# Kernel optimization log

Hardware: AMD Instinct MI355X
Metric: run time of the kernel (lower is better)

## Reference

```python
import jax, jax.numpy as jnp
import numpy as np

FULL_SCALE = 128.0
R = 0.5
TOPK = 4


def setup_inputs() -> dict:
    key = jax.random.key(0)
    k0, k1, k2, k3, k4 = jax.random.split(key, 5)
    B, Na, Nb, D = 16, 2048, 2048, 512
    coords_a = jax.random.randint(k0, (B, Na, 3), 0, 128, dtype=jnp.int32)
    coords_b = jax.random.randint(k1, (B, Nb, 3), 0, 128, dtype=jnp.int32)
    feats_a = jax.random.normal(k2, (B, Na, D), jnp.float32)
    feats_b = jax.random.normal(k3, (B, Nb, D), jnp.float32)
    W = jax.random.normal(k4, (2 * D, D), jnp.float32) / np.sqrt(2 * D).astype(np.float32)
    bias = jnp.zeros((D,), jnp.float32)
    return {"feats_a": feats_a, "feats_b": feats_b, "W": W, "bias": bias,
            "coords_a": coords_a, "coords_b": coords_b}


def _pairwise_l2(ca, cb):
    # ca: [B,Na,3], cb: [B,Nb,3] -> [B,Na,Nb], scaled by full_scale
    x2 = jnp.sum(ca * ca, axis=-1)[:, :, None]
    y2 = jnp.sum(cb * cb, axis=-1)[:, None, :]
    sq = x2 + y2 - 2.0 * jnp.einsum('bnd,bmd->bnm', ca, cb)
    return jnp.sqrt(jnp.clip(sq, 0.0, None)) / FULL_SCALE


def reference(feats_a, feats_b, W, bias, coords_a, coords_b):
    ca = coords_a.astype(jnp.float32)
    cb = coords_b.astype(jnp.float32)
    dist = _pairwise_l2(ca, cb)                       # [B,Na,Nb]
    neg_top, idx = jax.lax.top_k(-dist, TOPK)         # smallest TOPK distances
    dist_w = R - jnp.clip(-neg_top, 0.0, R)           # [B,Na,k]
    # gather neighbor features: [B,Na,k,D]
    b_f = jnp.take_along_axis(feats_b[:, None, :, :], idx[:, :, :, None], axis=2)
    a_f = feats_a[:, :, None, :]                      # broadcast over k
    h = jnp.concatenate([b_f, a_f - b_f], axis=-1)    # [B,Na,k,2D]
    fused = jnp.sum(jax.nn.relu(h @ W + bias) * dist_w[..., None], axis=2)  # [B,Na,D]
    # ME.cat(a, tmp): concatenate features along channel dim
    return jnp.concatenate([feats_a, fused], axis=-1)  # [B,Na,2D]
```

## Files before the change

kernel.cpp:

```cpp
#include <hip/hip_runtime.h>
#include <hip/hip_bf16.h>
#include <cstdint>
#include <cstddef>

#define NA   2048
#define NB   2048
#define DD   512

typedef __attribute__((ext_vector_type(8))) short bf16x8;
typedef __attribute__((ext_vector_type(4))) float f32x4;
typedef unsigned short u16;
typedef unsigned int   u32;

__device__ __forceinline__ u16 f2b_hw(float f) {
    u32 w;
    asm("v_cvt_pk_bf16_f32 %0, %1, %2" : "=v"(w) : "v"(f), "v"(f));
    return (u16)w;
}
__device__ __forceinline__ float b2f(u16 h) {
    return __uint_as_float(((u32)h) << 16);
}
__device__ __forceinline__ u32 umin32(u32 a, u32 b) { return a < b ? a : b; }
__device__ __forceinline__ u32 umax32(u32 a, u32 b) { return a > b ? a : b; }
__device__ __forceinline__ u32 med3u(u32 a, u32 b, u32 c) {
    return umax32(umin32(a, b), umin32(umax32(a, b), c));
}
__device__ __forceinline__ bf16x8 cvt8(f32x4 v0, f32x4 v1) {
    u32 w0, w1, w2, w3;
    asm("v_cvt_pk_bf16_f32 %0, %1, %2" : "=v"(w0) : "v"(v0[0]), "v"(v0[1]));
    asm("v_cvt_pk_bf16_f32 %0, %1, %2" : "=v"(w1) : "v"(v0[2]), "v"(v0[3]));
    asm("v_cvt_pk_bf16_f32 %0, %1, %2" : "=v"(w2) : "v"(v1[0]), "v"(v1[1]));
    asm("v_cvt_pk_bf16_f32 %0, %1, %2" : "=v"(w3) : "v"(v1[2]), "v"(v1[3]));
    union { u32 u[4]; bf16x8 v; } cv;
    cv.u[0] = w0; cv.u[1] = w1; cv.u[2] = w2; cv.u[3] = w3;
    return cv.v;
}

#define GLDS16(gsrc, ldst)                                                  \
    __builtin_amdgcn_global_load_lds(                                       \
        (const __attribute__((address_space(1))) void*)(gsrc),              \
        (__attribute__((address_space(3))) void*)(ldst), 16, 0, 0)

__global__ __launch_bounds__(256) void prep_w(const float* __restrict__ W,
                                              u16* __restrict__ W2T,
                                              u16* __restrict__ WdT) {
    __shared__ float s2[64][65];
    __shared__ float sd[64][65];
    int kb = blockIdx.x * 64, nb = blockIdx.y * 64;
    int tid = threadIdx.x;
    int c = tid & 63, r0 = tid >> 6;
    #pragma unroll
    for (int p = 0; p < 16; ++p) {
        int r = p * 4 + r0;
        float w1 = W[(size_t)(kb + r) * DD + nb + c];
        float w2 = W[(size_t)(512 + kb + r) * DD + nb + c];
        s2[r][c] = w2;
        sd[r][c] = w1 - w2;
    }
    __syncthreads();
    #pragma unroll
    for (int p = 0; p < 16; ++p) {
        int n = p * 4 + r0;
        W2T[(size_t)(nb + n) * DD + kb + c] = f2b_hw(s2[c][n]);
        WdT[(size_t)(nb + n) * DD + kb + c] = f2b_hw(sd[c][n]);
    }
}

__global__ __launch_bounds__(512) void topk_kernel(const int* __restrict__ ca,
                                                   const int* __restrict__ cb,
                                                   int* __restrict__ idx_out,
                                                   float* __restrict__ w_out) {
    __shared__ u32 pcb[NB];
    __shared__ u32 part[3 * 128 * 4];
    int b = blockIdx.y;
    int tid = threadIdx.x;
    for (int p = tid; p < NB; p += 512) {
        const int* c = cb + ((size_t)b * NB + p) * 3;
        pcb[p] = (u32)c[0] | ((u32)c[1] << 8) | ((u32)c[2] << 16);
    }
    __syncthreads();

    int q = tid & 127, g = tid >> 7;
    int i = blockIdx.x * 128 + q;
    const int* ac = ca + ((size_t)b * NA + i) * 3;
    int ax = ac[0], ay = ac[1], az = ac[2];

    u32 k0 = ~0u, k1 = ~0u, k2 = ~0u, k3 = ~0u;
    int j0 = g * 512;
    #pragma unroll 8
    for (int jj = 0; jj < 512; ++jj) {
        int j = j0 + jj;
        u32 p = pcb[j];
        int dx = ax - (int)(p & 255u);
        int dy = ay - (int)((p >> 8) & 255u);
        int dz = az - (int)(p >> 16);
        u32 s = (u32)(__mul24(dx, dx) + __mul24(dy, dy) + __mul24(dz, dz));
        u32 key = (s << 11) | (u32)j;
        u32 nk0 = umin32(k0, key);
        u32 nk1 = med3u(key, k0, k1);
        u32 nk2 = med3u(key, k1, k2);
        u32 nk3 = med3u(key, k2, k3);
        k0 = nk0; k1 = nk1; k2 = nk2; k3 = nk3;
    }
    if (g) {
        u32* pp = &part[((g - 1) * 128 + q) * 4];
        pp[0] = k0; pp[1] = k1; pp[2] = k2; pp[3] = k3;
    }
    __syncthreads();
    if (g == 0) {
        #pragma unroll
        for (int L = 0; L < 3; ++L) {
            const u32* pp = &part[(L * 128 + q) * 4];
            #pragma unroll
            for (int t = 0; t < 4; ++t) {
                u32 key = pp[t];
                u32 nk0 = umin32(k0, key);
                u32 nk1 = med3u(key, k0, k1);
                u32 nk2 = med3u(key, k1, k2);
                u32 nk3 = med3u(key, k2, k3);
                k0 = nk0; k1 = nk1; k2 = nk2; k3 = nk3;
            }
        }
        size_t o = ((size_t)b * NA + i) * 4;
        u32 ks[4] = {k0, k1, k2, k3};
        #pragma unroll
        for (int t = 0; t < 4; ++t) {
            idx_out[o + t] = (int)(ks[t] & 2047u);
            float d = sqrtf((float)(ks[t] >> 11)) * (1.0f / 128.0f);
            w_out[o + t] = 0.5f - fminf(d, 0.5f);
        }
    }
}

template<bool FUSED>
__global__ __launch_bounds__(256, 1) void gemm_kernel(
    const float* __restrict__ A, const u16* __restrict__ BT,
    u16* __restrict__ C, const int* __restrict__ idxb,
    const float* __restrict__ wb, const float* __restrict__ bias,
    const u16* __restrict__ Qb, float* __restrict__ out) {

    __shared__ __align__(16) char smem[FUSED ? 66560 : 65536];

    const int tid  = threadIdx.x;
    const int lane = tid & 63;
    const int wave = tid >> 6;
    const int mb   = blockIdx.x;
    const int m0   = FUSED ? ((((mb & 7) << 5) | (mb >> 3)) << 7) : (mb << 7);
    const int n0   = blockIdx.y << 8;
    const int l15  = lane & 15;
    const int fq   = lane >> 4;
    const int wr   = (wave >> 1) << 6;
    const int wc   = (wave & 1) << 7;

    int aflat[4]; const float* asp[4];
    #pragma unroll
    for (int i = 0; i < 4; ++i) {
        int flat = i * 256 + tid;
        int row = flat >> 3, pq = flat & 7;
        aflat[i] = flat;
        asp[i] = A + (size_t)(m0 + row) * DD + ((pq ^ (row & 7)) << 2);
    }
    int bflat[4]; const u16* bsp[4];
    #pragma unroll
    for (int i = 0; i < 4; ++i) {
        int flat = i * 256 + tid;
        int row = flat >> 2, pq = flat & 3;
        bflat[i] = flat;
        bsp[i] = BT + (size_t)(n0 + row) * DD + ((pq ^ ((row >> 1) & 3)) << 3);
    }

    int aoff[4][2], boff[8];
    #pragma unroll
    for (int mf = 0; mf < 4; ++mf) {
        int R = wr + mf * 16 + l15;
        aoff[mf][0] = R * 128 + (((2 * fq) ^ (R & 7)) << 4);
        aoff[mf][1] = R * 128 + (((2 * fq + 1) ^ (R & 7)) << 4);
    }
    #pragma unroll
    for (int nf = 0; nf < 8; ++nf) {
        int R = wc + nf * 16 + l15;
        boff[nf] = 16384 + R * 64 + ((fq ^ ((R >> 1) & 3)) << 4);
    }

    f32x4 acc[4][8];
    #pragma unroll
    for (int mf = 0; mf < 4; ++mf)
        #pragma unroll
        for (int nf = 0; nf < 8; ++nf)
            acc[mf][nf] = (f32x4){0.f, 0.f, 0.f, 0.f};

#define STAGE(kk, bufb)                                                      \
    { _Pragma("unroll") for (int i = 0; i < 4; ++i)                          \
          GLDS16(asp[i] + (kk), smem + (bufb) + aflat[i] * 16);              \
      _Pragma("unroll") for (int i = 0; i < 4; ++i)                          \
          GLDS16(bsp[i] + (kk), smem + (bufb) + 16384 + bflat[i] * 16); }

    STAGE(0, 0);

    #pragma unroll 1
    for (int t = 0; t < 16; ++t) {
        const int cur = (t & 1) * 32768;
        if (t < 15) {
            STAGE((t + 1) * 32, 32768 - cur);
            asm volatile("s_waitcnt vmcnt(8)" ::: "memory");
        } else {
            asm volatile("s_waitcnt vmcnt(0)" ::: "memory");
        }
        __builtin_amdgcn_s_barrier();

        bf16x8 af[4], bfr[8];
        #pragma unroll
        for (int mf = 0; mf < 4; ++mf) {
            f32x4 lo = *(const f32x4*)(smem + cur + aoff[mf][0]);
            f32x4 hi = *(const f32x4*)(smem + cur + aoff[mf][1]);
            af[mf] = cvt8(lo, hi);
        }
        #pragma unroll
        for (int nf = 0; nf < 8; ++nf)
            bfr[nf] = *(const bf16x8*)(smem + cur + boff[nf]);
        #pragma unroll
        for (int mf = 0; mf < 4; ++mf)
            #pragma unroll
            for (int nf = 0; nf < 8; ++nf)
                acc[mf][nf] = __builtin_amdgcn_mfma_f32_16x16x32_bf16(
                    af[mf], bfr[nf], acc[mf][nf], 0, 0, 0);

        __builtin_amdgcn_s_barrier();
    }

    const int r4 = (lane >> 4) * 4;

    if (!FUSED) {
        #pragma unroll
        for (int mf = 0; mf < 4; ++mf)
            #pragma unroll
            for (int nf = 0; nf < 8; ++nf)
                #pragma unroll
                for (int j = 0; j < 4; ++j) {
                    int row = m0 + wr + mf * 16 + r4 + j;
                    int col = n0 + wc + nf * 16 + l15;
                    C[(size_t)row * DD + col] = f2b_hw(acc[mf][nf][j]);
                }
        return;
    }

    {
        const float* src = A + (size_t)m0 * DD + n0;
        float*       dst = out + (size_t)m0 * 1024 + n0;
        #pragma unroll 4
        for (int it = 0; it < 32; ++it) {
            int flat = it * 256 + tid;
            int row = flat >> 6, qd = flat & 63;
            f32x4 v = *(const f32x4*)(src + (size_t)row * DD + qd * 4);
            *(f32x4*)(dst + (size_t)row * 1024 + qd * 4) = v;
        }
    }

    float bi[8];
    #pragma unroll
    for (int nf = 0; nf < 8; ++nf)
        bi[nf] = bias[n0 + wc + nf * 16 + l15];

    u16* Ps = (u16*)smem;
    #pragma unroll
    for (int mf = 0; mf < 4; ++mf)
        #pragma unroll
        for (int nf = 0; nf < 8; ++nf)
            #pragma unroll
            for (int j = 0; j < 4; ++j)
                Ps[(wr + mf * 16 + r4 + j) * 260 + wc + nf * 16 + l15] =
                    f2b_hw(acc[mf][nf][j] + bi[nf]);
    __syncthreads();

    const int g16 = tid >> 4, l16 = tid & 15;
    const u16* qs = Qb + ((size_t)(m0 >> 11) << 20);
    #pragma unroll
    for (int k = 0; k < 8; ++k) {
        const int r  = g16 * 8 + k;
        const int gr = m0 + r;
        int4  iv = *(const int4*)(idxb + (size_t)gr * 4);
        f32x4 wv = *(const f32x4*)(wb + (size_t)gr * 4);
        #pragma unroll
        for (int cc = 0; cc < 2; ++cc) {
            const int col = cc * 128 + l16 * 8;
            bf16x8 p8 = *(const bf16x8*)(Ps + r * 260 + col);
            bf16x8 q0 = *(const bf16x8*)(qs + (size_t)iv.x * DD + n0 + col);
            bf16x8 q1 = *(const bf16x8*)(qs + (size_t)iv.y * DD + n0 + col);
            bf16x8 q2 = *(const bf16x8*)(qs + (size_t)iv.z * DD + n0 + col);
            bf16x8 q3 = *(const bf16x8*)(qs + (size_t)iv.w * DD + n0 + col);
            float o[8];
            #pragma unroll
            for (int j = 0; j < 8; ++j) {
                float p = b2f((u16)p8[j]);
                float s;
                s  = fmaxf(p + b2f((u16)q0[j]), 0.f) * wv[0];
                s += fmaxf(p + b2f((u16)q1[j]), 0.f) * wv[1];
                s += fmaxf(p + b2f((u16)q2[j]), 0.f) * wv[2];
                s += fmaxf(p + b2f((u16)q3[j]), 0.f) * wv[3];
                o[j] = s;
            }
            float* op = out + (size_t)gr * 1024 + 512 + n0 + col;
            *(f32x4*)op       = (f32x4){o[0], o[1], o[2], o[3]};
            *(f32x4*)(op + 4) = (f32x4){o[4], o[5], o[6], o[7]};
        }
    }
}

extern "C" void kernel_launch(void* const* d_in, const int* in_sizes, int n_in,
                              void* d_out, int out_size, void* d_ws, size_t ws_size,
                              hipStream_t stream) {
    const float* fa   = (const float*)d_in[0];
    const float* fb   = (const float*)d_in[1];
    const float* W    = (const float*)d_in[2];
    const float* bias = (const float*)d_in[3];
    const int*   ca   = (const int*)d_in[4];
    const int*   cb   = (const int*)d_in[5];
    float* out = (float*)d_out;

    char* ws = (char*)d_ws;
    u16*   Qb   = (u16*)(ws);
    u16*   W2T  = (u16*)(ws + 33554432);
    u16*   WdT  = (u16*)(ws + 34078720);
    int*   idxb = (int*)(ws + 34603008);
    float* wb   = (float*)(ws + 35127296);

    dim3 pg(8, 8);
    prep_w<<<pg, 256, 0, stream>>>(W, W2T, WdT);

    dim3 tg(16, 16);
    topk_kernel<<<tg, 512, 0, stream>>>(ca, cb, idxb, wb);

    dim3 gg(256, 2);
    gemm_kernel<false><<<gg, 256, 0, stream>>>(fb, WdT, Qb, nullptr, nullptr,
                                               nullptr, nullptr, nullptr);
    gemm_kernel<true><<<gg, 256, 0, stream>>>(fa, W2T, nullptr, idxb, wb,
                                              bias, Qb, out);
}
```

Before: 138.4 us.

## Merge both GEMMs into one launch and split the gather epilogue into its own kernel

Both projection GEMMs (feats_b against WdT and feats_a against W2T) now run in a single 1024-block launch that writes bf16 P and Q buffers. A new lightweight epilogue kernel, with one wave per row, gathers the four neighbor Q rows, applies bias, ReLU and distance weights, and writes both halves of the output. The goal is to fill the GPU better by running the two GEMMs concurrently and to move the gather out of the GEMM's 1-block-per-CU occupancy. The cost is an extra bf16 P buffer written to and read back from global memory, plus one more kernel launch.

```diff
diff --git a/kernel.cpp b/kernel.cpp
--- a/kernel.cpp
+++ b/kernel.cpp
@@ -132,21 +132,25 @@
     }
 }
 
-template<bool FUSED>
-__global__ __launch_bounds__(256, 1) void gemm_kernel(
-    const float* __restrict__ A, const u16* __restrict__ BT,
-    u16* __restrict__ C, const int* __restrict__ idxb,
-    const float* __restrict__ wb, const float* __restrict__ bias,
-    const u16* __restrict__ Qb, float* __restrict__ out) {
-
-    __shared__ __align__(16) char smem[FUSED ? 66560 : 65536];
+__global__ __launch_bounds__(256, 1) void gemm_qp(
+    const float* __restrict__ fa, const float* __restrict__ fb,
+    const u16* __restrict__ W2T, const u16* __restrict__ WdT,
+    u16* __restrict__ Pb, u16* __restrict__ Qb) {
+
+    __shared__ __align__(16) char smem[65536];
+
+    const int bid  = blockIdx.x;
+    const int half = bid >> 9;
+    const int idx  = bid & 511;
+    const float* A  = half ? fa : fb;
+    const u16*   BT = half ? W2T : WdT;
+    u16*         C  = half ? Pb : Qb;
 
     const int tid  = threadIdx.x;
     const int lane = tid & 63;
     const int wave = tid >> 6;
-    const int mb   = blockIdx.x;
-    const int m0   = FUSED ? ((((mb & 7) << 5) | (mb >> 3)) << 7) : (mb << 7);
-    const int n0   = blockIdx.y << 8;
+    const int m0   = (idx >> 1) << 7;
+    const int n0   = (idx & 1) << 8;
     const int l15  = lane & 15;
     const int fq   = lane >> 4;
     const int wr   = (wave >> 1) << 6;
@@ -229,81 +233,73 @@
     }
 
     const int r4 = (lane >> 4) * 4;
-
-    if (!FUSED) {
-        #pragma unroll
-        for (int mf = 0; mf < 4; ++mf)
-            #pragma unroll
-            for (int nf = 0; nf < 8; ++nf)
-                #pragma unroll
-                for (int j = 0; j < 4; ++j) {
-                    int row = m0 + wr + mf * 16 + r4 + j;
-                    int col = n0 + wc + nf * 16 + l15;
-                    C[(size_t)row * DD + col] = f2b_hw(acc[mf][nf][j]);
-                }
-        return;
-    }
-
-    {
-        const float* src = A + (size_t)m0 * DD + n0;
-        float*       dst = out + (size_t)m0 * 1024 + n0;
-        #pragma unroll 4
-        for (int it = 0; it < 32; ++it) {
-            int flat = it * 256 + tid;
-            int row = flat >> 6, qd = flat & 63;
-            f32x4 v = *(const f32x4*)(src + (size_t)row * DD + qd * 4);
-            *(f32x4*)(dst + (size_t)row * 1024 + qd * 4) = v;
-        }
-    }
-
-    float bi[8];
-    #pragma unroll
-    for (int nf = 0; nf < 8; ++nf)
-        bi[nf] = bias[n0 + wc + nf * 16 + l15];
-
-    u16* Ps = (u16*)smem;
     #pragma unroll
     for (int mf = 0; mf < 4; ++mf)
         #pragma unroll
         for (int nf = 0; nf < 8; ++nf)
             #pragma unroll
-            for (int j = 0; j < 4; ++j)
-                Ps[(wr + mf * 16 + r4 + j) * 260 + wc + nf * 16 + l15] =
-                    f2b_hw(acc[mf][nf][j] + bi[nf]);
-    __syncthreads();
-
-    const int g16 = tid >> 4, l16 = tid & 15;
-    const u16* qs = Qb + ((size_t)(m0 >> 11) << 20);
-    #pragma unroll
-    for (int k = 0; k < 8; ++k) {
-        const int r  = g16 * 8 + k;
-        const int gr = m0 + r;
-        int4  iv = *(const int4*)(idxb + (size_t)gr * 4);
-        f32x4 wv = *(const f32x4*)(wb + (size_t)gr * 4);
-        #pragma unroll
-        for (int cc = 0; cc < 2; ++cc) {
-            const int col = cc * 128 + l16 * 8;
-            bf16x8 p8 = *(const bf16x8*)(Ps + r * 260 + col);
-            bf16x8 q0 = *(const bf16x8*)(qs + (size_t)iv.x * DD + n0 + col);
-            bf16x8 q1 = *(const bf16x8*)(qs + (size_t)iv.y * DD + n0 + col);
-            bf16x8 q2 = *(const bf16x8*)(qs + (size_t)iv.z * DD + n0 + col);
-            bf16x8 q3 = *(const bf16x8*)(qs + (size_t)iv.w * DD + n0 + col);
-            float o[8];
-            #pragma unroll
-            for (int j = 0; j < 8; ++j) {
-                float p = b2f((u16)p8[j]);
-                float s;
-                s  = fmaxf(p + b2f((u16)q0[j]), 0.f) * wv[0];
-                s += fmaxf(p + b2f((u16)q1[j]), 0.f) * wv[1];
-                s += fmaxf(p + b2f((u16)q2[j]), 0.f) * wv[2];
-                s += fmaxf(p + b2f((u16)q3[j]), 0.f) * wv[3];
-                o[j] = s;
+            for (int j = 0; j < 4; ++j) {
+                int row = m0 + wr + mf * 16 + r4 + j;
+                int col = n0 + wc + nf * 16 + l15;
+                C[(size_t)row * DD + col] = f2b_hw(acc[mf][nf][j]);
             }
-            float* op = out + (size_t)gr * 1024 + 512 + n0 + col;
-            *(f32x4*)op       = (f32x4){o[0], o[1], o[2], o[3]};
-            *(f32x4*)(op + 4) = (f32x4){o[4], o[5], o[6], o[7]};
-        }
-    }
+}
+
+__global__ __launch_bounds__(256) void epilogue_kernel(
+    const float* __restrict__ fa, const u16* __restrict__ Pb,
+    const u16* __restrict__ Qb, const int* __restrict__ idxb,
+    const float* __restrict__ wb, const float* __restrict__ bias,
+    float* __restrict__ out) {
+
+    int bid = blockIdx.x;
+    int ob  = (bid & 7) * 1024 + (bid >> 3);
+    int tid  = threadIdx.x;
+    int r    = ob * 4 + (tid >> 6);
+    int lane = tid & 63;
+    int c8   = lane * 8;
+    int b    = r >> 11;
+
+    const int*   ip = idxb + (size_t)r * 4;
+    const float* wp = wb + (size_t)r * 4;
+    int   i0 = ip[0], i1 = ip[1], i2 = ip[2], i3 = ip[3];
+    float w0 = wp[0], w1 = wp[1], w2 = wp[2], w3 = wp[3];
+
+    const float* ar = fa + (size_t)r * DD + c8;
+    f32x4 a0 = *(const f32x4*)ar;
+    f32x4 a1 = *(const f32x4*)(ar + 4);
+
+    bf16x8 pv = *(const bf16x8*)(Pb + (size_t)r * DD + c8);
+    f32x4 bia0 = *(const f32x4*)(bias + c8);
+    f32x4 bia1 = *(const f32x4*)(bias + c8 + 4);
+
+    size_t qbase = ((size_t)b << 11) * DD;
+    bf16x8 qv0 = *(const bf16x8*)(Qb + qbase + (size_t)i0 * DD + c8);
+    bf16x8 qv1 = *(const bf16x8*)(Qb + qbase + (size_t)i1 * DD + c8);
+    bf16x8 qv2 = *(const bf16x8*)(Qb + qbase + (size_t)i2 * DD + c8);
+    bf16x8 qv3 = *(const bf16x8*)(Qb + qbase + (size_t)i3 * DD + c8);
+
+    float base[8], acc[8];
+    #pragma unroll
+    for (int j = 0; j < 8; ++j) {
+        float bj = (j < 4) ? bia0[j] : bia1[j - 4];
+        base[j] = b2f((u16)pv[j]) + bj;
+        acc[j] = 0.f;
+    }
+    #pragma unroll
+    for (int j = 0; j < 8; ++j) {
+        acc[j] += fmaxf(base[j] + b2f((u16)qv0[j]), 0.f) * w0;
+        acc[j] += fmaxf(base[j] + b2f((u16)qv1[j]), 0.f) * w1;
+        acc[j] += fmaxf(base[j] + b2f((u16)qv2[j]), 0.f) * w2;
+        acc[j] += fmaxf(base[j] + b2f((u16)qv3[j]), 0.f) * w3;
+    }
+
+    float* orow = out + (size_t)r * 1024;
+    *(f32x4*)(orow + c8)     = a0;
+    *(f32x4*)(orow + c8 + 4) = a1;
+    f32x4 o0 = {acc[0], acc[1], acc[2], acc[3]};
+    f32x4 o1 = {acc[4], acc[5], acc[6], acc[7]};
+    *(f32x4*)(orow + 512 + c8)     = o0;
+    *(f32x4*)(orow + 512 + c8 + 4) = o1;
 }
 
 extern "C" void kernel_launch(void* const* d_in, const int* in_sizes, int n_in,
@@ -319,10 +315,11 @@
 
     char* ws = (char*)d_ws;
     u16*   Qb   = (u16*)(ws);
-    u16*   W2T  = (u16*)(ws + 33554432);
-    u16*   WdT  = (u16*)(ws + 34078720);
-    int*   idxb = (int*)(ws + 34603008);
-    float* wb   = (float*)(ws + 35127296);
+    u16*   Pb   = (u16*)(ws + 33554432);
+    u16*   W2T  = (u16*)(ws + 67108864);
+    u16*   WdT  = (u16*)(ws + 67633152);
+    int*   idxb = (int*)(ws + 68157440);
+    float* wb   = (float*)(ws + 68681728);
 
     dim3 pg(8, 8);
     prep_w<<<pg, 256, 0, stream>>>(W, W2T, WdT);
@@ -330,9 +327,7 @@
     dim3 tg(16, 16);
     topk_kernel<<<tg, 512, 0, stream>>>(ca, cb, idxb, wb);
 
-    dim3 gg(256, 2);
-    gemm_kernel<false><<<gg, 256, 0, stream>>>(fb, WdT, Qb, nullptr, nullptr,
-                                               nullptr, nullptr, nullptr);
-    gemm_kernel<true><<<gg, 256, 0, stream>>>(fa, W2T, nullptr, idxb, wb,
-                                              bias, Qb, out);
-}
+    gemm_qp<<<1024, 256, 0, stream>>>(fa, fb, W2T, WdT, Pb, Qb);
+
+    epilogue_kernel<<<8192, 256, 0, stream>>>(fa, Pb, Qb, idxb, wb, bias, out);
+}
```

After: 148.4 us. +7.2%, slower.
